# Kernel tuning notes

Measured on AMD Instinct MI355X. Metric: run time of the kernel, lower is better.

The kernel has to match this reference:

```python
import jax, jax.numpy as jnp
import numpy as np

B, L, DIM, H = 2, 2048, 1024, 16
HD = DIM // H  # head dim = 64
MASK_SCALE = -10 * 6  # faithful to the original source: mask_expand *= -10 * 6


def setup_inputs() -> dict:
    key = jax.random.key(0)
    ks = jax.random.split(key, 8)
    s = 1.0 / np.sqrt(DIM)
    return {
        "x": jax.random.normal(ks[0], (B, L, DIM), jnp.float32),
        "attention_mask": jax.random.uniform(ks[1], (B, L, L), jnp.float32),
        "Wq": jax.random.normal(ks[2], (DIM, DIM), jnp.float32) * s,
        "bq": jnp.zeros((DIM,), jnp.float32),
        "Wk": jax.random.normal(ks[3], (DIM, DIM), jnp.float32) * s,
        "bk": jnp.zeros((DIM,), jnp.float32),
        "Wv": jax.random.normal(ks[4], (DIM, DIM), jnp.float32) * s,
        "bv": jnp.zeros((DIM,), jnp.float32),
    }


def _split_heads(t):
    # [B, L, DIM] -> [B, H, L, HD]
    return t.reshape(B, L, H, HD).transpose(0, 2, 1, 3)


def reference(x, attention_mask, Wq, bq, Wk, bk, Wv, bv):
    q = _split_heads(x @ Wq + bq)
    k = _split_heads(x @ Wk + bk)
    v = _split_heads(x @ Wv + bv)
    scale = float(HD) ** -0.5
    # full [B, H, L, L] score matrix, as in the original
    scores = jnp.einsum("bhqd,bhkd->bhqk", q, k) * scale
    scores = scores + attention_mask[:, None, :, :] * MASK_SCALE
    probs = jax.nn.softmax(scores, axis=-1)
    ctx = jnp.einsum("bhqk,bhkd->bhqd", probs, v)
    # merge heads back: [B, L, DIM]
    return ctx.transpose(0, 2, 1, 3).reshape(B, L, DIM)
```

## Files before the change

kernel.cpp:

```cpp
#include <hip/hip_runtime.h>

#define LL 2048
#define NHEADS 16
#define HDIM 64
#define QSCALE 0.18033688011112042f
#define MASKC1 -86.56170245333780f

typedef __attribute__((ext_vector_type(8))) __bf16 bf16x8;
typedef __attribute__((ext_vector_type(4))) float f32x4;
typedef __attribute__((ext_vector_type(4))) unsigned int u32x4;

__device__ __forceinline__ unsigned short f2bf(float f) {
  unsigned int u = __builtin_bit_cast(unsigned int, f);
  u += 0x7fffu + ((u >> 16) & 1u);
  return (unsigned short)(u >> 16);
}

__device__ __forceinline__ bf16x8 ld_frag(const unsigned short* p) {
  return *reinterpret_cast<const bf16x8*>(p);
}

__device__ __forceinline__ float bflo(unsigned int u) {
  return __builtin_bit_cast(float, u << 16);
}
__device__ __forceinline__ float bfhi(unsigned int u) {
  return __builtin_bit_cast(float, u & 0xffff0000u);
}
__device__ __forceinline__ unsigned int pack2(float hi, float lo) {
  return __builtin_amdgcn_perm(__builtin_bit_cast(unsigned int, hi),
                               __builtin_bit_cast(unsigned int, lo), 0x07060302u);
}

__device__ __forceinline__ void async_cp16(const unsigned short* g, unsigned short* l) {
  __builtin_amdgcn_global_load_lds(
      (const __attribute__((address_space(1))) unsigned int*)(unsigned long long)(g),
      (__attribute__((address_space(3))) unsigned int*)(unsigned int)(unsigned long long)(l),
      16, 0, 0);
}

__device__ __forceinline__ void lem_load(const unsigned short* p, uint4& a, uint4& b,
                                         uint4& c, uint4& d) {
  asm volatile("global_load_dwordx4 %0, %4, off\n\t"
               "global_load_dwordx4 %1, %4, off offset:16\n\t"
               "global_load_dwordx4 %2, %4, off offset:32\n\t"
               "global_load_dwordx4 %3, %4, off offset:48"
               : "=&v"(a), "=&v"(b), "=&v"(c), "=&v"(d)
               : "v"(p)
               : "memory");
}

__global__ __launch_bounds__(256) void cvt_x_kernel(const float* __restrict__ x,
                                                    unsigned short* __restrict__ xb) {
  int i = (blockIdx.x * 256 + threadIdx.x) * 4;
  float4 v = *reinterpret_cast<const float4*>(x + i);
  ushort4 o;
  o.x = f2bf(v.x); o.y = f2bf(v.y); o.z = f2bf(v.z); o.w = f2bf(v.w);
  *reinterpret_cast<ushort4*>(xb + i) = o;
}

__global__ __launch_bounds__(256) void transpose_w_kernel(const float* __restrict__ Wq,
                                                          const float* __restrict__ Wk,
                                                          const float* __restrict__ Wv,
                                                          unsigned short* __restrict__ WtAll) {
  int z = blockIdx.z;
  const float* W = (z == 0) ? Wq : (z == 1) ? Wk : Wv;
  unsigned short* dst = WtAll + (size_t)z * 1024 * 1024;
  int n0 = blockIdx.x * 64, k0 = blockIdx.y * 64;
  __shared__ float t[64][65];
  int tx = threadIdx.x & 63, ty = threadIdx.x >> 6;
#pragma unroll
  for (int p = 0; p < 16; ++p) {
    int kr = p * 4 + ty;
    t[kr][tx] = W[(size_t)(k0 + kr) * 1024 + n0 + tx];
  }
  __syncthreads();
#pragma unroll
  for (int p = 0; p < 16; ++p) {
    int nr = p * 4 + ty;
    dst[(size_t)(n0 + nr) * 1024 + k0 + tx] = f2bf(t[tx][nr]);
  }
}

__global__ __launch_bounds__(256) void lem_prep_kernel(const float* __restrict__ mask,
                                                       unsigned short* __restrict__ lem) {
  const int qb = blockIdx.x, kt = blockIdx.y, b = blockIdx.z;
  const int tid = threadIdx.x;
  __shared__ unsigned short lds[128 * 72];
  {
    const int r0 = tid >> 4;
    const int c0 = (tid & 15) * 4;
#pragma unroll
    for (int p = 0; p < 8; ++p) {
      int row = p * 16 + r0;
      float4 v = *reinterpret_cast<const float4*>(
          mask + ((size_t)b * LL + qb * 128 + row) * LL + kt * 64 + c0);
      ushort4 o;
      o.x = f2bf(v.x * MASKC1); o.y = f2bf(v.y * MASKC1);
      o.z = f2bf(v.z * MASKC1); o.w = f2bf(v.w * MASKC1);
      *reinterpret_cast<ushort4*>(&lds[row * 72 + c0]) = o;
    }
  }
  __syncthreads();
  const int w = tid >> 6, lane = tid & 63, g = lane >> 4, cc = lane & 15;
  unsigned int ow[16];
#pragma unroll
  for (int mt = 0; mt < 2; ++mt) {
    const int q = w * 32 + mt * 16 + cc;
#pragma unroll
    for (int nt = 0; nt < 4; ++nt) {
      uint2 v = *reinterpret_cast<const uint2*>(&lds[q * 72 + nt * 16 + g * 4]);
      ow[mt * 8 + nt * 2]     = v.x;
      ow[mt * 8 + nt * 2 + 1] = v.y;
    }
  }
  uint4* dst = reinterpret_cast<uint4*>(
      lem + ((((size_t)b * 16 + qb) * 32 + kt) * 256 + tid) * 32);
#pragma unroll
  for (int j = 0; j < 4; ++j)
    dst[j] = make_uint4(ow[4 * j], ow[4 * j + 1], ow[4 * j + 2], ow[4 * j + 3]);
}

__global__ __launch_bounds__(256) void qkv_gemm_kernel(
    const unsigned short* __restrict__ xb, const unsigned short* __restrict__ WtAll,
    const float* __restrict__ bq, const float* __restrict__ bk, const float* __restrict__ bv,
    unsigned short* __restrict__ qkv) {
  const int z = blockIdx.z;
  const unsigned short* Wt = WtAll + (size_t)z * 1024 * 1024;
  const float* bias = (z == 0) ? bq : (z == 1) ? bk : bv;
  unsigned short* outb = qkv + (size_t)z * 4194304;

  __shared__ __align__(16) unsigned short smem[16384];
  unsigned short* As = smem;
  unsigned short* Bs = smem + 8192;

  const int tid = threadIdx.x;
  const int w = tid >> 6, lane = tid & 63, g = lane >> 4, cc = lane & 15;
  const int wm = w >> 1, wn = w & 1;
  const int m0 = blockIdx.y * 128, n0 = blockIdx.x * 128;
  const int srow = lane >> 3;
  const int gc = ((lane & 7) - srow) & 7;
  const unsigned short* ga = xb + (size_t)(m0 + w * 32 + srow) * 1024 + gc * 8;
  const unsigned short* gb = Wt + (size_t)(n0 + w * 32 + srow) * 1024 + gc * 8;
  unsigned short* la = As + w * 2048;
  unsigned short* lb = Bs + w * 2048;

  f32x4 acc[4][4];
#pragma unroll
  for (int i = 0; i < 4; ++i)
#pragma unroll
    for (int j = 0; j < 4; ++j) acc[i][j] = (f32x4)0.0f;

  for (int kk = 0; kk < 1024; kk += 64) {
    __syncthreads();
#pragma unroll
    for (int i = 0; i < 4; ++i) {
      async_cp16(ga + i * 8192 + kk, la + i * 512);
      async_cp16(gb + i * 8192 + kk, lb + i * 512);
    }
    __syncthreads();
    bf16x8 af[4][2], bfr[4][2];
#pragma unroll
    for (int mt = 0; mt < 4; ++mt)
#pragma unroll
      for (int ks = 0; ks < 2; ++ks)
        af[mt][ks] = ld_frag(&As[(wm * 64 + mt * 16 + cc) * 64 + ((4 * ks + g + cc) & 7) * 8]);
#pragma unroll
    for (int nt = 0; nt < 4; ++nt)
#pragma unroll
      for (int ks = 0; ks < 2; ++ks)
        bfr[nt][ks] = ld_frag(&Bs[(wn * 64 + nt * 16 + cc) * 64 + ((4 * ks + g + cc) & 7) * 8]);
#pragma unroll
    for (int mt = 0; mt < 4; ++mt)
#pragma unroll
      for (int nt = 0; nt < 4; ++nt)
#pragma unroll
        for (int ks = 0; ks < 2; ++ks)
          acc[mt][nt] = __builtin_amdgcn_mfma_f32_16x16x32_bf16(af[mt][ks], bfr[nt][ks],
                                                                acc[mt][nt], 0, 0, 0);
  }

  if (z != 2) {
    const float sc = (z == 0) ? QSCALE : 1.0f;
#pragma unroll
    for (int nt = 0; nt < 4; ++nt) {
      int n = n0 + wn * 64 + nt * 16 + cc;
      float bval = bias[n];
      int h = n >> 6, d = n & 63;
#pragma unroll
      for (int mt = 0; mt < 4; ++mt) {
#pragma unroll
        for (int r = 0; r < 4; ++r) {
          int m = m0 + wm * 64 + mt * 16 + g * 4 + r;
          int b = m >> 11, l = m & 2047;
          outb[(((size_t)(b * NHEADS + h) * LL) + l) * HDIM + d] =
              f2bf((acc[mt][nt][r] + bval) * sc);
        }
      }
    }
  } else {
    __syncthreads();
#pragma unroll
    for (int nt = 0; nt < 4; ++nt) {
      int nr = wn * 64 + nt * 16 + cc;
      float bval = bias[n0 + nr];
#pragma unroll
      for (int mt = 0; mt < 4; ++mt)
#pragma unroll
        for (int r = 0; r < 4; ++r)
          smem[nr * 128 + wm * 64 + (mt >> 1) * 32 + g * 8 + (mt & 1) * 4 + r] =
              f2bf(acc[mt][nt][r] + bval);
    }
    __syncthreads();
    int row = tid >> 1, half = tid & 1;
    int n = n0 + row, hh = n >> 6, dd = n & 63;
    int bb = m0 >> 11, l0 = (m0 & 2047) + half * 64;
    unsigned short* dst = outb + ((size_t)(bb * NHEADS + hh) * HDIM + dd) * LL + l0;
#pragma unroll
    for (int i = 0; i < 8; ++i)
      *reinterpret_cast<uint4*>(dst + i * 8) =
          *reinterpret_cast<const uint4*>(&smem[row * 128 + half * 64 + i * 8]);
  }
}

__global__ __launch_bounds__(256, 2) void flash_kernel(
    const unsigned short* __restrict__ Qb, const unsigned short* __restrict__ Kb,
    const unsigned short* __restrict__ Vt, const unsigned short* __restrict__ Lem,
    float* __restrict__ out) {
  const int id = blockIdx.y * 16 + blockIdx.x;
  const int nid = (id & 7) * 64 + (id >> 3);
  const int qb = nid & 15, bh = nid >> 4;
  const int b = bh >> 4, h = bh & 15;
  const int q0 = qb * 128;
  const int tid = threadIdx.x, w = tid >> 6, lane = tid & 63, g = lane >> 4, cc = lane & 15;
  const size_t bhoff = (size_t)bh * LL * HDIM;

  __shared__ __align__(16) unsigned short Ks[3][64 * 64];
  __shared__ __align__(16) unsigned short Vs[3][64 * 64];

  bf16x8 aq[2][2];
#pragma unroll
  for (int mt = 0; mt < 2; ++mt)
#pragma unroll
    for (int ks = 0; ks < 2; ++ks)
      aq[mt][ks] = *reinterpret_cast<const bf16x8*>(
          Qb + bhoff + (size_t)(q0 + w * 32 + mt * 16 + cc) * HDIM + ks * 32 + g * 8);

  const int srow = lane >> 3;
  const int gcs = ((lane & 7) - srow) & 7;
  const unsigned short* kg0 = Kb + bhoff + (size_t)(w * 8 + srow) * HDIM + gcs * 8;
  const unsigned short* kg1 = Kb + bhoff + (size_t)(32 + w * 8 + srow) * HDIM + gcs * 8;
  const unsigned short* vg0 = Vt + bhoff + (size_t)(w * 8 + srow) * LL + gcs * 8;
  const unsigned short* vg1 = Vt + bhoff + (size_t)(32 + w * 8 + srow) * LL + gcs * 8;

  const unsigned short* lemq = Lem + (((size_t)b * 16 + qb) * 32 * 256 + tid) * 32;

  const u32x4 onesu = {0x3F803F80u, 0x3F803F80u, 0x3F803F80u, 0x3F803F80u};
  const bf16x8 bones = __builtin_bit_cast(bf16x8, onesu);

  uint4 l00, l01, l02, l03, l10, l11, l12, l13, l20, l21, l22, l23;

  f32x4 liacc[2];
  f32x4 oacc[2][4];
#pragma unroll
  for (int mt = 0; mt < 2; ++mt) {
    liacc[mt] = (f32x4)0.0f;
#pragma unroll
    for (int nt = 0; nt < 4; ++nt) oacc[mt][nt] = (f32x4)0.0f;
  }

  async_cp16(kg0, Ks[0] + w * 512);
  async_cp16(kg1, Ks[0] + (w + 4) * 512);
  async_cp16(vg0, Vs[0] + w * 512);
  async_cp16(vg1, Vs[0] + (w + 4) * 512);
  lem_load(lemq, l00, l01, l02, l03);
  lemq += 8192;
  async_cp16(kg0 + (size_t)64 * HDIM, Ks[1] + w * 512);
  async_cp16(kg1 + (size_t)64 * HDIM, Ks[1] + (w + 4) * 512);
  async_cp16(vg0 + 64, Vs[1] + w * 512);
  async_cp16(vg1 + 64, Vs[1] + (w + 4) * 512);
  lem_load(lemq, l10, l11, l12, l13);
  lemq += 8192;

#define FLASH_COMPUTE(BUF, LSA, LSB, LSC, LSD)                                         \
  {                                                                                    \
    bf16x8 bk_[4][2], bv[4][2];                                                        \
    _Pragma("unroll") for (int nt = 0; nt < 4; ++nt)                                   \
      _Pragma("unroll") for (int ks = 0; ks < 2; ++ks)                                 \
        bk_[nt][ks] =                                                                  \
            ld_frag(&Ks[BUF][(nt * 16 + cc) * 64 + ((4 * ks + g + cc) & 7) * 8]);      \
    _Pragma("unroll") for (int nt = 0; nt < 4; ++nt)                                   \
      _Pragma("unroll") for (int ks = 0; ks < 2; ++ks)                                 \
        bv[nt][ks] =                                                                   \
            ld_frag(&Vs[BUF][(nt * 16 + cc) * 64 + ((4 * ks + g + cc) & 7) * 8]);      \
    bf16x8 ap[2][2];                                                                   \
    _Pragma("unroll") for (int mt = 0; mt < 2; ++mt) {                                 \
      f32x4 sacc[4];                                                                   \
      const uint4 ea = (mt == 0) ? LSA : LSC;                                          \
      const uint4 eb = (mt == 0) ? LSB : LSD;                                          \
      sacc[0][0] = bflo(ea.x); sacc[0][1] = bfhi(ea.x);                                \
      sacc[0][2] = bflo(ea.y); sacc[0][3] = bfhi(ea.y);                                \
      sacc[1][0] = bflo(ea.z); sacc[1][1] = bfhi(ea.z);                                \
      sacc[1][2] = bflo(ea.w); sacc[1][3] = bfhi(ea.w);                                \
      sacc[2][0] = bflo(eb.x); sacc[2][1] = bfhi(eb.x);                                \
      sacc[2][2] = bflo(eb.y); sacc[2][3] = bfhi(eb.y);                                \
      sacc[3][0] = bflo(eb.z); sacc[3][1] = bfhi(eb.z);                                \
      sacc[3][2] = bflo(eb.w); sacc[3][3] = bfhi(eb.w);                                \
      _Pragma("unroll") for (int nt = 0; nt < 4; ++nt)                                 \
        _Pragma("unroll") for (int ks = 0; ks < 2; ++ks)                               \
          sacc[nt] = __builtin_amdgcn_mfma_f32_16x16x32_bf16(bk_[nt][ks], aq[mt][ks],  \
                                                             sacc[nt], 0, 0, 0);       \
      float p[4][4];                                                                   \
      _Pragma("unroll") for (int nt = 0; nt < 4; ++nt)                                 \
        _Pragma("unroll") for (int r = 0; r < 4; ++r)                                  \
          p[nt][r] = __builtin_amdgcn_exp2f(sacc[nt][r]);                              \
      unsigned int wd[8];                                                              \
      _Pragma("unroll") for (int ks = 0; ks < 2; ++ks) {                               \
        wd[ks * 4 + 0] = pack2(p[2 * ks][1],     p[2 * ks][0]);                        \
        wd[ks * 4 + 1] = pack2(p[2 * ks][3],     p[2 * ks][2]);                        \
        wd[ks * 4 + 2] = pack2(p[2 * ks + 1][1], p[2 * ks + 1][0]);                    \
        wd[ks * 4 + 3] = pack2(p[2 * ks + 1][3], p[2 * ks + 1][2]);                    \
        u32x4 uv = {wd[ks * 4], wd[ks * 4 + 1], wd[ks * 4 + 2], wd[ks * 4 + 3]};       \
        ap[mt][ks] = __builtin_bit_cast(bf16x8, uv);                                   \
      }                                                                                \
    }                                                                                  \
    _Pragma("unroll") for (int mt = 0; mt < 2; ++mt) {                                 \
      _Pragma("unroll") for (int nt = 0; nt < 4; ++nt)                                 \
        _Pragma("unroll") for (int ks = 0; ks < 2; ++ks)                               \
          oacc[mt][nt] = __builtin_amdgcn_mfma_f32_16x16x32_bf16(ap[mt][ks], bv[nt][ks],\
                                                                 oacc[mt][nt], 0, 0, 0);\
      _Pragma("unroll") for (int ks = 0; ks < 2; ++ks)                                 \
        liacc[mt] = __builtin_amdgcn_mfma_f32_16x16x32_bf16(ap[mt][ks], bones,         \
                                                            liacc[mt], 0, 0, 0);       \
    }                                                                                  \
  }

#define FITER(KT, CBUF, SBUF, VMC, ISSUE, UA, UB, UC, UD, LA, LB, LC, LD)              \
  {                                                                                    \
    asm volatile("s_waitcnt vmcnt(" VMC ")" ::: "memory");                             \
    __builtin_amdgcn_sched_barrier(0);                                                 \
    asm volatile("s_barrier" ::: "memory");                                            \
    __builtin_amdgcn_sched_barrier(0);                                                 \
    if (ISSUE) {                                                                       \
      const size_t ko = (size_t)((KT) + 2) * 64;                                       \
      async_cp16(kg0 + ko * HDIM, Ks[SBUF] + w * 512);                                 \
      async_cp16(kg1 + ko * HDIM, Ks[SBUF] + (w + 4) * 512);                           \
      async_cp16(vg0 + ko, Vs[SBUF] + w * 512);                                        \
      async_cp16(vg1 + ko, Vs[SBUF] + (w + 4) * 512);                                  \
      lem_load(lemq, LA, LB, LC, LD);                                                  \
      lemq += 8192;                                                                    \
    }                                                                                  \
    FLASH_COMPUTE(CBUF, UA, UB, UC, UD);                                               \
  }

  for (int kt = 0; kt < 30; kt += 3) {
    FITER(kt + 0, 0, 2, "8", true,  l00, l01, l02, l03, l20, l21, l22, l23)
    FITER(kt + 1, 1, 0, "8", true,  l10, l11, l12, l13, l00, l01, l02, l03)
    FITER(kt + 2, 2, 1, "8", true,  l20, l21, l22, l23, l10, l11, l12, l13)
  }
  FITER(30, 0, 0, "8", false, l00, l01, l02, l03, l00, l01, l02, l03)
  FITER(31, 1, 0, "0", false, l10, l11, l12, l13, l10, l11, l12, l13)

#undef FITER
#undef FLASH_COMPUTE

#pragma unroll
  for (int mt = 0; mt < 2; ++mt) {
#pragma unroll
    for (int r = 0; r < 4; ++r) {
      float inv = 1.0f / liacc[mt][r];
      int qrow = q0 + w * 32 + mt * 16 + g * 4 + r;
#pragma unroll
      for (int nt = 0; nt < 4; ++nt)
        out[((size_t)b * LL + qrow) * 1024 + h * 64 + nt * 16 + cc] = oacc[mt][nt][r] * inv;
    }
  }
}

extern "C" void kernel_launch(void* const* d_in, const int* in_sizes, int n_in,
                              void* d_out, int out_size, void* d_ws, size_t ws_size,
                              hipStream_t stream) {
  const float* x    = (const float*)d_in[0];
  const float* mask = (const float*)d_in[1];
  const float* Wq   = (const float*)d_in[2];
  const float* bq   = (const float*)d_in[3];
  const float* Wk   = (const float*)d_in[4];
  const float* bk   = (const float*)d_in[5];
  const float* Wv   = (const float*)d_in[6];
  const float* bv   = (const float*)d_in[7];
  float* out = (float*)d_out;
  (void)in_sizes; (void)n_in; (void)out_size; (void)ws_size;

  char* ws = (char*)d_ws;
  unsigned short* qkv = (unsigned short*)(ws);
  unsigned short* xb  = (unsigned short*)(ws + (24u << 20));
  unsigned short* Wt  = (unsigned short*)(ws + (32u << 20));
  unsigned short* lem = (unsigned short*)(ws + (24u << 20));

  cvt_x_kernel<<<dim3(4096), dim3(256), 0, stream>>>(x, xb);
  transpose_w_kernel<<<dim3(16, 16, 3), dim3(256), 0, stream>>>(Wq, Wk, Wv, Wt);
  qkv_gemm_kernel<<<dim3(8, 32, 3), dim3(256), 0, stream>>>(xb, Wt, bq, bk, bv, qkv);
  lem_prep_kernel<<<dim3(16, 32, 2), dim3(256), 0, stream>>>(mask, lem);
  flash_kernel<<<dim3(16, 32), dim3(256), 0, stream>>>(qkv, qkv + 4194304, qkv + 8388608,
                                                       lem, out);
}
```

Before: 201.2 us.

## Triple-buffer QKV GEMM LDS with async prefetch two tiles ahead

```diff
diff --git a/kernel.cpp b/kernel.cpp
--- a/kernel.cpp
+++ b/kernel.cpp
@@ -129,20 +129,29 @@
   const float* bias = (z == 0) ? bq : (z == 1) ? bk : bv;
   unsigned short* outb = qkv + (size_t)z * 4194304;
 
-  __shared__ __align__(16) unsigned short smem[16384];
-  unsigned short* As = smem;
-  unsigned short* Bs = smem + 8192;
+  __shared__ __align__(16) unsigned short smem[24576];
 
   const int tid = threadIdx.x;
   const int w = tid >> 6, lane = tid & 63, g = lane >> 4, cc = lane & 15;
   const int wm = w >> 1, wn = w & 1;
   const int m0 = blockIdx.y * 128, n0 = blockIdx.x * 128;
-  const int srow = lane >> 3;
-  const int gc = ((lane & 7) - srow) & 7;
-  const unsigned short* ga = xb + (size_t)(m0 + w * 32 + srow) * 1024 + gc * 8;
-  const unsigned short* gb = Wt + (size_t)(n0 + w * 32 + srow) * 1024 + gc * 8;
-  unsigned short* la = As + w * 2048;
-  unsigned short* lb = Bs + w * 2048;
+
+  const int prl = lane >> 3, sl = lane & 7;
+  int r0g, c0g, r1g, c1g;
+  {
+    int pr0 = w * 16 + prl;       int j0 = (sl - pr0) & 7;
+    r0g = 2 * pr0 + (j0 >> 2);    c0g = j0 & 3;
+    int pr1 = w * 16 + 8 + prl;   int j1 = (sl - pr1) & 7;
+    r1g = 2 * pr1 + (j1 >> 2);    c1g = j1 & 3;
+  }
+  const unsigned short* gaA0 = xb + (size_t)(m0 + r0g) * 1024 + c0g * 8;
+  const unsigned short* gaA1 = xb + (size_t)(m0 + r1g) * 1024 + c1g * 8;
+  const unsigned short* gbB0 = Wt + (size_t)(n0 + r0g) * 1024 + c0g * 8;
+  const unsigned short* gbB1 = Wt + (size_t)(n0 + r1g) * 1024 + c1g * 8;
+
+  const int praB = wm * 32 + (cc >> 1);
+  const int prbB = wn * 32 + (cc >> 1);
+  const int sab = ((cc >> 1) + (cc & 1) * 4 + g) & 7;
 
   f32x4 acc[4][4];
 #pragma unroll
@@ -150,34 +159,51 @@
 #pragma unroll
     for (int j = 0; j < 4; ++j) acc[i][j] = (f32x4)0.0f;
 
-  for (int kk = 0; kk < 1024; kk += 64) {
-    __syncthreads();
-#pragma unroll
-    for (int i = 0; i < 4; ++i) {
-      async_cp16(ga + i * 8192 + kk, la + i * 512);
-      async_cp16(gb + i * 8192 + kk, lb + i * 512);
-    }
-    __syncthreads();
-    bf16x8 af[4][2], bfr[4][2];
-#pragma unroll
-    for (int mt = 0; mt < 4; ++mt)
-#pragma unroll
-      for (int ks = 0; ks < 2; ++ks)
-        af[mt][ks] = ld_frag(&As[(wm * 64 + mt * 16 + cc) * 64 + ((4 * ks + g + cc) & 7) * 8]);
-#pragma unroll
-    for (int nt = 0; nt < 4; ++nt)
-#pragma unroll
-      for (int ks = 0; ks < 2; ++ks)
-        bfr[nt][ks] = ld_frag(&Bs[(wn * 64 + nt * 16 + cc) * 64 + ((4 * ks + g + cc) & 7) * 8]);
-#pragma unroll
-    for (int mt = 0; mt < 4; ++mt)
-#pragma unroll
-      for (int nt = 0; nt < 4; ++nt)
-#pragma unroll
-        for (int ks = 0; ks < 2; ++ks)
-          acc[mt][nt] = __builtin_amdgcn_mfma_f32_16x16x32_bf16(af[mt][ks], bfr[nt][ks],
-                                                                acc[mt][nt], 0, 0, 0);
-  }
+  async_cp16(gaA0, smem + w * 1024);
+  async_cp16(gaA1, smem + w * 1024 + 512);
+  async_cp16(gbB0, smem + 12288 + w * 1024);
+  async_cp16(gbB1, smem + 12288 + w * 1024 + 512);
+  async_cp16(gaA0 + 32, smem + 4096 + w * 1024);
+  async_cp16(gaA1 + 32, smem + 4096 + w * 1024 + 512);
+  async_cp16(gbB0 + 32, smem + 12288 + 4096 + w * 1024);
+  async_cp16(gbB1 + 32, smem + 12288 + 4096 + w * 1024 + 512);
+
+#define GITER(KT, CBUF, SBUF, VMC, ISSUE)                                              \
+  {                                                                                    \
+    asm volatile("s_waitcnt vmcnt(" VMC ")" ::: "memory");                             \
+    __builtin_amdgcn_sched_barrier(0);                                                 \
+    asm volatile("s_barrier" ::: "memory");                                            \
+    __builtin_amdgcn_sched_barrier(0);                                                 \
+    if (ISSUE) {                                                                       \
+      async_cp16(gaA0 + ((KT) + 2) * 32, smem + (SBUF) * 4096 + w * 1024);             \
+      async_cp16(gaA1 + ((KT) + 2) * 32, smem + (SBUF) * 4096 + w * 1024 + 512);       \
+      async_cp16(gbB0 + ((KT) + 2) * 32, smem + 12288 + (SBUF) * 4096 + w * 1024);     \
+      async_cp16(gbB1 + ((KT) + 2) * 32, smem + 12288 + (SBUF) * 4096 + w * 1024 + 512);\
+    }                                                                                  \
+    {                                                                                  \
+      const unsigned short* Ab = smem + (CBUF) * 4096;                                 \
+      const unsigned short* Bb = smem + 12288 + (CBUF) * 4096;                         \
+      bf16x8 af[4], bfr[4];                                                            \
+      _Pragma("unroll") for (int mt = 0; mt < 4; ++mt)                                 \
+        af[mt] = ld_frag(&Ab[(praB + 8 * mt) * 64 + sab * 8]);                         \
+      _Pragma("unroll") for (int nt = 0; nt < 4; ++nt)                                 \
+        bfr[nt] = ld_frag(&Bb[(prbB + 8 * nt) * 64 + sab * 8]);                        \
+      _Pragma("unroll") for (int mt = 0; mt < 4; ++mt)                                 \
+        _Pragma("unroll") for (int nt = 0; nt < 4; ++nt)                               \
+          acc[mt][nt] = __builtin_amdgcn_mfma_f32_16x16x32_bf16(af[mt], bfr[nt],       \
+                                                                acc[mt][nt], 0, 0, 0); \
+    }                                                                                  \
+  }
+
+  for (int kt = 0; kt < 30; kt += 3) {
+    GITER(kt + 0, 0, 2, "4", true)
+    GITER(kt + 1, 1, 0, "4", true)
+    GITER(kt + 2, 2, 1, "4", true)
+  }
+  GITER(30, 0, 0, "4", false)
+  GITER(31, 1, 0, "0", false)
+
+#undef GITER
 
   if (z != 2) {
     const float sc = (z == 0) ? QSCALE : 1.0f;
```

Result: faster. 193.9 us (-3.6%).
